# Kernel optimization log

Hardware: AMD Instinct MI355X
Metric: run time of the kernel (lower is better)

The kernel has to match this reference:

```python
import jax, jax.numpy as jnp
import numpy as np
from jax import lax

SQRT_HALF = np.float32(np.sqrt(0.5))


def glu_block(x, pad_mask, w, b):
    # x: [B,T,D], pad_mask: [B,T] True=padded, w: [2D,D,3], b: [2D]
    x = jnp.where(pad_mask[..., None], 0.0, x)
    xc = jnp.transpose(x, (0, 2, 1))  # [B,D,T]
    y = lax.conv_general_dilated(xc, w, (1,), 'SAME',
                                 dimension_numbers=('NCH', 'OIH', 'NCH'))
    y = y + b[None, :, None]
    y = jnp.transpose(y, (0, 2, 1))  # [B,T,2D]
    a, g = jnp.split(y, 2, axis=-1)
    out = a * jax.nn.sigmoid(g)
    return (out + x) * SQRT_HALF


def setup_inputs() -> dict:
    key = jax.random.key(0)
    ks = jax.random.split(key, 12)
    B, T_MEL, T_PH, D, V, MEL_D = 32, 2000, 512, 256, 100, 80
    mels = jax.random.normal(ks[0], (B, T_MEL, MEL_D), dtype=jnp.float32)
    phonemes = jax.random.randint(ks[1], (B, T_PH), 0, V)
    mel_lens = jax.random.randint(ks[2], (B,), 1, T_MEL)
    phoneme_lens = jax.random.randint(ks[3], (B,), 1, T_PH)
    embedding = 0.02 * jax.random.normal(ks[4], (V, D), dtype=jnp.float32)
    mel_conv_w = 0.02 * jax.random.normal(ks[5], (D, MEL_D, 3), dtype=jnp.float32)
    mel_conv_b = jnp.zeros((D,), dtype=jnp.float32)
    ph_w = 0.02 * jax.random.normal(ks[6], (4, 2 * D, D, 3), dtype=jnp.float32)
    ph_b = jnp.zeros((4, 2 * D), dtype=jnp.float32)
    mel_w = 0.02 * jax.random.normal(ks[7], (4, 2 * D, D, 3), dtype=jnp.float32)
    mel_b = jnp.zeros((4, 2 * D), dtype=jnp.float32)
    return {"mels": mels, "phonemes": phonemes, "mel_lens": mel_lens,
            "phoneme_lens": phoneme_lens, "embedding": embedding,
            "mel_conv_w": mel_conv_w, "mel_conv_b": mel_conv_b,
            "ph_w": ph_w, "ph_b": ph_b, "mel_w": mel_w, "mel_b": mel_b}


def reference(mels, phonemes, mel_lens, phoneme_lens, embedding,
              mel_conv_w, mel_conv_b, ph_w, ph_b, mel_w, mel_b):
    B, T_mel, _ = mels.shape
    # --- mel encoder ---
    mel_mask = jnp.arange(T_mel)[None, :] >= mel_lens[:, None]  # [B,T_mel]
    mc = lax.conv_general_dilated(jnp.transpose(mels, (0, 2, 1)), mel_conv_w,
                                  (1,), 'SAME',
                                  dimension_numbers=('NCH', 'OIH', 'NCH'))
    mel_enc = jnp.transpose(mc + mel_conv_b[None, :, None], (0, 2, 1))
    for i in range(4):
        mel_enc = glu_block(mel_enc, mel_mask, mel_w[i], mel_b[i])
    # --- phoneme encoder (prepend blank index 0) ---
    ph = jnp.pad(phonemes, ((0, 0), (1, 0)), constant_values=0)  # [B,T_ph+1]
    T_ph1 = ph.shape[1]
    ph_mask = jnp.arange(T_ph1)[None, :] > phoneme_lens[:, None]  # [B,T_ph+1]
    ph_enc = embedding[ph]  # [B,T_ph+1,D]
    for i in range(4):
        ph_enc = glu_block(ph_enc, ph_mask, ph_w[i], ph_b[i])
    # --- negative squared pairwise L2 distances, masked over padded phonemes ---
    mel_sq = jnp.sum(mel_enc * mel_enc, axis=-1)  # [B,T_mel]
    ph_sq = jnp.sum(ph_enc * ph_enc, axis=-1)     # [B,T_ph+1]
    dots = jnp.einsum('btd,bsd->bts', mel_enc, ph_enc)  # [B,T_mel,T_ph+1]
    distances = 2.0 * dots - mel_sq[:, :, None] - ph_sq[:, None, :]
    distances = jnp.where(ph_mask[:, None, :], -1e9, distances)
    attn = jax.nn.softmax(distances, axis=2)
    context = jnp.einsum('bts,bsd->btd', attn, ph_enc)
    return jnp.concatenate([mel_enc, context], axis=2)  # [B,T_mel,2D]
```

## Files before the change

### kernel.cpp

```cpp
#include <hip/hip_runtime.h>

typedef _Float16 f16;
typedef __attribute__((ext_vector_type(8))) _Float16 half8;
typedef __attribute__((ext_vector_type(4))) _Float16 half4;
typedef __attribute__((ext_vector_type(4))) float f32x4;

__device__ inline f32x4 mfma16(half8 a, half8 b, f32x4 c) {
  return __builtin_amdgcn_mfma_f32_16x16x32_f16(a, b, c, 0, 0, 0);
}

__global__ void prep_wtglu_kernel(const float* __restrict__ mel_w,
                                  const float* __restrict__ ph_w,
                                  f16* __restrict__ wt) {
  int bid = blockIdx.x;
  int l = bid >> 9, r = bid & 511;
  int tid = threadIdx.x;
  int n32 = r >> 5, j = r & 31;
  int ch = (j < 16) ? (n32 * 16 + j) : (256 + n32 * 16 + (j - 16));
  const float* src = ((l < 4) ? (mel_w + (size_t)l * 512 * 256 * 3)
                              : (ph_w + (size_t)(l - 4) * 512 * 256 * 3)) +
                     (size_t)ch * 768;
  f16* dst = wt + (size_t)bid * 768;
  float a0 = src[tid * 3], a1 = src[tid * 3 + 1], a2 = src[tid * 3 + 2];
  dst[tid] = (f16)a0;
  dst[256 + tid] = (f16)a1;
  dst[512 + tid] = (f16)a2;
}

__global__ void prep_wt0_kernel(const float* __restrict__ w, f16* __restrict__ wt0) {
  int idx = blockIdx.x * 256 + threadIdx.x;
  const int total = 256 * 288;
  if (idx >= total) return;
  int o = idx / 288, k = idx % 288;
  int tap = k / 96, i = k % 96;
  wt0[idx] = (i < 80) ? (f16)w[((size_t)o * 80 + i) * 3 + tap] : (f16)0.f;
}

__global__ void embed_kernel(const int* __restrict__ phon, const float* __restrict__ emb,
                             f16* __restrict__ out) {
  int s = blockIdx.x, b = blockIdx.y;
  int lane = threadIdx.x;
  int tok = (s == 0) ? 0 : phon[b * 512 + (s - 1)];
  float4 f = *(const float4*)(emb + (size_t)tok * 256 + lane * 4);
  half4 h = {(f16)f.x, (f16)f.y, (f16)f.z, (f16)f.w};
  *(half4*)(out + ((size_t)b * 513 + s) * 256 + lane * 4) = h;
}

__global__ __launch_bounds__(256) void conv0_kernel(
    const float* __restrict__ mels, const f16* __restrict__ wt0,
    const float* __restrict__ bias, f16* __restrict__ out) {
  __shared__ f16 xs[66 * 104];
  __shared__ f16 ws[64 * 104];
  const int tid = threadIdx.x;
  const int b = blockIdx.z;
  const int t0 = blockIdx.x * 64;
  const int by = blockIdx.y;

  for (int idx = tid; idx < 66 * 24; idx += 256) {
    int r = idx / 24, v = idx % 24;
    int t = t0 - 1 + r;
    half4 h = {0.f, 0.f, 0.f, 0.f};
    if (t >= 0 && t < 2000 && v < 20) {
      float4 f = *(const float4*)(mels + ((size_t)b * 2000 + t) * 80 + v * 4);
      h[0] = (f16)f.x; h[1] = (f16)f.y; h[2] = (f16)f.z; h[3] = (f16)f.w;
    }
    *(half4*)(xs + r * 104 + v * 4) = h;
  }
  const int lane = tid & 63, wv = tid >> 6;
  const int wr = wv >> 1, wc = wv & 1;
  const int l15 = lane & 15, q = lane >> 4;
  f32x4 acc[2][2] = {};
  const f16* wrow = wt0 + (size_t)(by * 64) * 288;
  for (int tap = 0; tap < 3; ++tap) {
    __syncthreads();
    for (int idx = tid; idx < 64 * 12; idx += 256) {
      int r = idx / 12, v = idx % 12;
      *(half8*)(ws + r * 104 + v * 8) =
          *(const half8*)(wrow + (size_t)r * 288 + tap * 96 + v * 8);
    }
    __syncthreads();
#pragma unroll
    for (int s2 = 0; s2 < 3; ++s2) {
      int ch = s2 * 32 + q * 8;
      half8 a0 = *(const half8*)(xs + (32 * wr + l15 + tap) * 104 + ch);
      half8 a1 = *(const half8*)(xs + (32 * wr + 16 + l15 + tap) * 104 + ch);
      half8 b0 = *(const half8*)(ws + (32 * wc + l15) * 104 + ch);
      half8 b1 = *(const half8*)(ws + (32 * wc + 16 + l15) * 104 + ch);
      acc[0][0] = mfma16(a0, b0, acc[0][0]);
      acc[0][1] = mfma16(a0, b1, acc[0][1]);
      acc[1][0] = mfma16(a1, b0, acc[1][0]);
      acc[1][1] = mfma16(a1, b1, acc[1][1]);
    }
  }
#pragma unroll
  for (int rf = 0; rf < 2; ++rf)
#pragma unroll
    for (int cf = 0; cf < 2; ++cf) {
      int c = by * 64 + 32 * wc + 16 * cf + l15;
      float bb = bias[c];
#pragma unroll
      for (int r = 0; r < 4; ++r) {
        int t = t0 + 32 * wr + 16 * rf + 4 * q + r;
        if (t < 2000)
          out[((size_t)b * 2000 + t) * 256 + c] = (f16)(acc[rf][cf][r] + bb);
      }
    }
}

__device__ __forceinline__ void glu_body(
    f16* xs, f16* ws2,
    const f16* __restrict__ x, const f16* __restrict__ wt,
    const float* __restrict__ bias, f16* __restrict__ out,
    const int* __restrict__ lens, int lenAdd, int T, int TT, int writeConst,
    int bx, int by, int b) {
  const int tid = threadIdx.x;
  const int tt = (bx + b) % TT;
  const int t0 = tt * 128;
  int thr = lens[b] + lenAdd;
  if (thr > T) thr = T;
  const size_t xbase = (size_t)b * T * 256;
  const int lane = tid & 63, wv = tid >> 6;
  const int wr = wv >> 1, wc = wv & 1;
  const int l15 = lane & 15, q = lane >> 4;

  if (t0 > thr) {
    if (writeConst) {
#pragma unroll
      for (int p = 0; p < 2; ++p) {
        int n32 = by * 4 + wc * 2 + p;
        int c = n32 * 16 + l15;
        float ba = bias[c], bg = bias[256 + c];
        f16 o = (f16)((ba * (1.0f / (1.0f + __expf(-bg)))) * 0.70710678118f);
#pragma unroll
        for (int mt = 0; mt < 4; ++mt)
#pragma unroll
          for (int rr = 0; rr < 4; ++rr) {
            int t = t0 + wr * 64 + mt * 16 + q * 4 + rr;
            if (t < T) out[xbase + (size_t)t * 256 + c] = o;
          }
      }
    }
    return;
  }

  f32x4 acc[4][4] = {};
  const f16* wrow = wt + (size_t)(by * 128) * 768;
  const int r_st = tid >> 3, v_st = tid & 7;

  half8 xr[5], wreg[4];
  auto loadX = [&](int cb) {
#pragma unroll
    for (int it = 0; it < 5; ++it) {
      int idx = tid + it * 256;
      half8 val = {};
      if (idx < 1040) {
        int lr = idx >> 3, v = idx & 7;
        int trow = t0 - 1 + lr;
        if (trow >= 0 && trow < thr)
          val = *(const half8*)(x + xbase + (size_t)trow * 256 + cb * 64 + v * 8);
      }
      xr[it] = val;
    }
  };
  auto storeX = [&]() {
#pragma unroll
    for (int it = 0; it < 5; ++it) {
      int idx = tid + it * 256;
      if (idx < 1040) {
        int lr = idx >> 3, v = idx & 7;
        *(half8*)(xs + lr * 72 + v * 8) = xr[it];
      }
    }
  };
  auto loadW = [&](int tap, int cb) {
#pragma unroll
    for (int it = 0; it < 4; ++it) {
      int r = r_st + 32 * it;
      wreg[it] = *(const half8*)(wrow + (size_t)r * 768 + tap * 256 + cb * 64 + v_st * 8);
    }
  };
  auto storeW = [&]() {
#pragma unroll
    for (int it = 0; it < 4; ++it)
      *(half8*)(ws2 + (r_st + 32 * it) * 72 + v_st * 8) = wreg[it];
  };

  loadX(0);
  loadW(0, 0);

  for (int p = 0; p < 12; ++p) {
    const int cb = p / 3, tap = p - cb * 3;
    __syncthreads();
    if (tap == 0) storeX();
    storeW();
    __syncthreads();
    if (p < 11) {
      int np = p + 1, ncb = np / 3, ntap = np - ncb * 3;
      if (ntap == 0) loadX(ncb);
      loadW(ntap, ncb);
    }

    half8 af[4][2];
#pragma unroll
    for (int mt = 0; mt < 4; ++mt)
#pragma unroll
      for (int kc = 0; kc < 2; ++kc)
        af[mt][kc] = *(const half8*)(xs + (wr * 64 + mt * 16 + l15 + tap) * 72 + kc * 32 + q * 8);
#pragma unroll
    for (int nt = 0; nt < 4; ++nt) {
      half8 b0 = *(const half8*)(ws2 + (wc * 64 + nt * 16 + l15) * 72 + q * 8);
      half8 b1 = *(const half8*)(ws2 + (wc * 64 + nt * 16 + l15) * 72 + 32 + q * 8);
#pragma unroll
      for (int mt = 0; mt < 4; ++mt) {
        acc[mt][nt] = mfma16(af[mt][0], b0, acc[mt][nt]);
        acc[mt][nt] = mfma16(af[mt][1], b1, acc[mt][nt]);
      }
    }
  }

#pragma unroll
  for (int p = 0; p < 2; ++p) {
    int n32 = by * 4 + wc * 2 + p;
    int c = n32 * 16 + l15;
    float ba = bias[c], bg = bias[256 + c];
#pragma unroll
    for (int mt = 0; mt < 4; ++mt) {
#pragma unroll
      for (int rr = 0; rr < 4; ++rr) {
        int t = t0 + wr * 64 + mt * 16 + q * 4 + rr;
        if (t < T && (writeConst || t < thr)) {
          float a = acc[mt][2 * p][rr] + ba;
          float g = acc[mt][2 * p + 1][rr] + bg;
          float xm = (t < thr) ? (float)x[xbase + (size_t)t * 256 + c] : 0.f;
          float o = (a * (1.0f / (1.0f + __expf(-g))) + xm) * 0.70710678118f;
          out[xbase + (size_t)t * 256 + c] = (f16)o;
        }
      }
    }
  }
}

__global__ __launch_bounds__(256) void glu_fused_kernel(
    const f16* __restrict__ xm, const f16* __restrict__ wtm,
    const float* __restrict__ bm, f16* __restrict__ om,
    const int* __restrict__ mlens,
    const f16* __restrict__ xp, const f16* __restrict__ wtp,
    const float* __restrict__ bp, f16* __restrict__ op,
    const int* __restrict__ plens, int writeConst) {
  __shared__ f16 xs[132 * 72];
  __shared__ f16 ws2[128 * 72];
  const int lin = blockIdx.x;
  if (lin < 2048) {
    int b = lin >> 6, y = (lin >> 4) & 3, x = lin & 15;
    glu_body(xs, ws2, xm, wtm, bm, om, mlens, 0, 2000, 16, writeConst, x, y, b);
  } else {
    int l2 = lin - 2048;
    int b = l2 / 20, r = l2 % 20, y = r / 5, x = r % 5;
    glu_body(xs, ws2, xp, wtp, bp, op, plens, 1, 513, 5, writeConst, x, y, b);
  }
}

__global__ __launch_bounds__(256) void transpose_kernel(const f16* __restrict__ ph,
                                                        f16* __restrict__ phT) {
  __shared__ f16 tile[64 * 72];
  const int tid = threadIdx.x;
  const int b = blockIdx.z, s0 = blockIdx.x * 64, d0 = blockIdx.y * 64;
#pragma unroll
  for (int it = 0; it < 2; ++it) {
    int idx = tid + it * 256;
    int r = idx >> 3, v = idx & 7;
    int s = s0 + r;
    half8 val = {};
    if (s < 513) val = *(const half8*)(ph + ((size_t)b * 513 + s) * 256 + d0 + v * 8);
    *(half8*)(tile + r * 72 + v * 8) = val;
  }
  __syncthreads();
#pragma unroll
  for (int it = 0; it < 2; ++it) {
    int idx = tid + it * 256;
    int r = idx >> 3, v = idx & 7;
    half8 val;
#pragma unroll
    for (int j2 = 0; j2 < 8; ++j2) val[j2] = tile[(v * 8 + j2) * 72 + r];
    *(half8*)(phT + ((size_t)b * 256 + d0 + r) * 576 + s0 + v * 8) = val;
  }
}

__global__ void sqnorm_kernel(const f16* __restrict__ x, float* __restrict__ sq, int nrows) {
  int row = blockIdx.x * 4 + (threadIdx.x >> 6);
  int lane = threadIdx.x & 63;
  if (row >= nrows) return;
  const f16* p = x + (size_t)row * 256;
  float v = 0.f;
  for (int i = lane; i < 256; i += 64) { float f = (float)p[i]; v += f * f; }
  for (int off = 32; off > 0; off >>= 1) v += __shfl_down(v, off);
  if (lane == 0) sq[row] = v;
}

__global__ __launch_bounds__(256) void flash_kernel(
    const f16* __restrict__ mel, const f16* __restrict__ ph,
    const f16* __restrict__ phT, const float* __restrict__ phsq,
    const int* __restrict__ plens, float* __restrict__ out) {
  __shared__ f16 vt[256 * 72];
  __shared__ f16 ps[4][16 * 72];
  __shared__ float phs[576];
  const int tid = threadIdx.x;
  const int lin = blockIdx.x;
  const int b = ((lin >> 8) << 3) | (lin & 7);
  const int t0 = ((lin >> 3) & 31) * 64;
  const int lane = tid & 63, wv = tid >> 6;
  const int l15 = lane & 15, q = lane >> 4;
  const int plen = plens[b];
  const int nkt = (plen + 64) >> 6;

  for (int idx = tid; idx < 576; idx += 256)
    phs[idx] = (idx < 513) ? phsq[b * 513 + idx] : 0.f;

  const int tq = t0 + 16 * wv + l15;
  half8 qf[8];
  {
    const f16* qrow = mel + ((size_t)b * 2000 + ((tq < 2000) ? tq : 0)) * 256;
#pragma unroll
    for (int c = 0; c < 8; ++c) qf[c] = *(const half8*)(qrow + c * 32 + q * 8);
    if (tq >= 2000) {
      half8 z = {};
#pragma unroll
      for (int c = 0; c < 8; ++c) qf[c] = z;
    }
  }
  if (tq < 2000) {
    float* orow = out + ((size_t)b * 2000 + tq) * 512;
#pragma unroll
    for (int c = 0; c < 8; ++c) {
      half8 h = qf[c];
      float4 f0 = {(float)h[0], (float)h[1], (float)h[2], (float)h[3]};
      float4 f1 = {(float)h[4], (float)h[5], (float)h[6], (float)h[7]};
      *(float4*)(orow + c * 32 + q * 8) = f0;
      *(float4*)(orow + c * 32 + q * 8 + 4) = f1;
    }
  }

  half8 vreg[8];
  const int d_st = tid >> 3, v_st = tid & 7;
  auto loadV = [&](int kt) {
#pragma unroll
    for (int it = 0; it < 8; ++it) {
      int d = d_st + 32 * it;
      vreg[it] = *(const half8*)(phT + ((size_t)b * 256 + d) * 576 + kt * 64 + v_st * 8);
    }
  };
  loadV(0);

  float mr[4], lr[4];
#pragma unroll
  for (int r = 0; r < 4; ++r) { mr[r] = -3.0e38f; lr[r] = 0.f; }
  f32x4 acc[16] = {};
  f16* pw = ps[wv];

#pragma unroll 1
  for (int kt = 0; kt < nkt; ++kt) {
    const int s0 = kt * 64;
    __syncthreads();
#pragma unroll
    for (int it = 0; it < 8; ++it)
      *(half8*)(vt + (d_st + 32 * it) * 72 + v_st * 8) = vreg[it];
    __syncthreads();
    if (kt + 1 < nkt) loadV(kt + 1);

    const f16* krow[4];
#pragma unroll
    for (int cf = 0; cf < 4; ++cf)
      krow[cf] = ph + ((size_t)b * 513 + (s0 + cf * 16 + l15)) * 256 + q * 8;
    f32x4 sc[4] = {};
    __builtin_amdgcn_s_setprio(1);
#pragma unroll
    for (int c = 0; c < 8; ++c) {
#pragma unroll
      for (int cf = 0; cf < 4; ++cf) {
        half8 bf = *(const half8*)(krow[cf] + c * 32);
        sc[cf] = mfma16(qf[c], bf, sc[cf]);
      }
    }
    __builtin_amdgcn_s_setprio(0);
    float p[4][4];
    float rmax[4] = {-3.0e38f, -3.0e38f, -3.0e38f, -3.0e38f};
#pragma unroll
    for (int cf = 0; cf < 4; ++cf) {
      int sloc = cf * 16 + l15;
      int s = s0 + sloc;
      bool msk = (s > plen) || (s >= 513);
      float p2 = phs[s0 + sloc];
#pragma unroll
      for (int r = 0; r < 4; ++r) {
        float v = 2.0f * sc[cf][r] - p2;
        if (msk) v = -1.0e9f;
        p[cf][r] = v;
        rmax[r] = fmaxf(rmax[r], v);
      }
    }
#pragma unroll
    for (int r = 0; r < 4; ++r)
#pragma unroll
      for (int off = 1; off < 16; off <<= 1)
        rmax[r] = fmaxf(rmax[r], __shfl_xor(rmax[r], off));
    float alpha[4];
#pragma unroll
    for (int r = 0; r < 4; ++r) {
      float mn = fmaxf(mr[r], rmax[r]);
      alpha[r] = __expf(mr[r] - mn);
      mr[r] = mn;
      float rs = 0.f;
#pragma unroll
      for (int cf = 0; cf < 4; ++cf) {
        float e = __expf(p[cf][r] - mn);
        p[cf][r] = e;
        rs += e;
      }
#pragma unroll
      for (int off = 1; off < 16; off <<= 1) rs += __shfl_xor(rs, off);
      lr[r] = lr[r] * alpha[r] + rs;
    }
#pragma unroll
    for (int dt = 0; dt < 16; ++dt)
#pragma unroll
      for (int r = 0; r < 4; ++r) acc[dt][r] *= alpha[r];
#pragma unroll
    for (int cf = 0; cf < 4; ++cf)
#pragma unroll
      for (int r = 0; r < 4; ++r)
        pw[(q * 4 + r) * 72 + cf * 16 + l15] = (f16)p[cf][r];
#pragma unroll
    for (int kc = 0; kc < 2; ++kc) {
      half8 pa = *(const half8*)(pw + l15 * 72 + kc * 32 + q * 8);
      __builtin_amdgcn_s_setprio(1);
#pragma unroll
      for (int dt = 0; dt < 16; ++dt) {
        half8 vb = *(const half8*)(vt + (dt * 16 + l15) * 72 + kc * 32 + q * 8);
        acc[dt] = mfma16(pa, vb, acc[dt]);
      }
      __builtin_amdgcn_s_setprio(0);
    }
  }
  float inv[4];
#pragma unroll
  for (int r = 0; r < 4; ++r) inv[r] = 1.0f / lr[r];
#pragma unroll
  for (int dt = 0; dt < 16; ++dt)
#pragma unroll
    for (int r = 0; r < 4; ++r) {
      int t = t0 + 16 * wv + q * 4 + r;
      if (t < 2000) {
        int d = dt * 16 + l15;
        out[((size_t)b * 2000 + t) * 512 + 256 + d] = acc[dt][r] * inv[r];
      }
    }
}

extern "C" void kernel_launch(void* const* d_in, const int* in_sizes, int n_in,
                              void* d_out, int out_size, void* d_ws, size_t ws_size,
                              hipStream_t stream) {
  (void)in_sizes; (void)n_in; (void)out_size; (void)ws_size;
  const float* mels       = (const float*)d_in[0];
  const int*   phonemes   = (const int*)d_in[1];
  const int*   mel_lens   = (const int*)d_in[2];
  const int*   ph_lens    = (const int*)d_in[3];
  const float* embedding  = (const float*)d_in[4];
  const float* mel_conv_w = (const float*)d_in[5];
  const float* mel_conv_b = (const float*)d_in[6];
  const float* ph_w       = (const float*)d_in[7];
  const float* ph_b       = (const float*)d_in[8];
  const float* mel_w      = (const float*)d_in[9];
  const float* mel_b      = (const float*)d_in[10];
  float* out = (float*)d_out;

  char* wsp = (char*)d_ws;
  size_t off = 0;
  auto alloc = [&](size_t bytes) -> void* {
    void* p = wsp + off;
    off = (off + bytes + 255) & ~(size_t)255;
    return p;
  };
  f16* wtg    = (f16*)alloc(8ull * 512 * 768 * 2);
  f16* wt0    = (f16*)alloc(256ull * 288 * 2);
  float* phsq = (float*)alloc(16416ull * 4);
  f16* p0     = (f16*)alloc(32ull * 513 * 256 * 2);
  f16* p1     = (f16*)alloc(32ull * 513 * 256 * 2);
  f16* m0     = (f16*)alloc(32ull * 2000 * 256 * 2);
  f16* m1     = (f16*)alloc(32ull * 2000 * 256 * 2);
  f16* phT = m1;

  prep_wtglu_kernel<<<4096, 256, 0, stream>>>(mel_w, ph_w, wtg);
  prep_wt0_kernel<<<288, 256, 0, stream>>>(mel_conv_w, wt0);
  embed_kernel<<<dim3(513, 32), 64, 0, stream>>>(phonemes, embedding, p0);
  conv0_kernel<<<dim3(32, 4, 32), 256, 0, stream>>>(mels, wt0, mel_conv_b, m0);

  const size_t WL = 512ull * 768;
  glu_fused_kernel<<<2688, 256, 0, stream>>>(
      m0, wtg + 0 * WL, mel_b + 0 * 512, m1, mel_lens,
      p0, wtg + 4 * WL, ph_b + 0 * 512, p1, ph_lens, 0);
  glu_fused_kernel<<<2688, 256, 0, stream>>>(
      m1, wtg + 1 * WL, mel_b + 1 * 512, m0, mel_lens,
      p1, wtg + 5 * WL, ph_b + 1 * 512, p0, ph_lens, 0);
  glu_fused_kernel<<<2688, 256, 0, stream>>>(
      m0, wtg + 2 * WL, mel_b + 2 * 512, m1, mel_lens,
      p0, wtg + 6 * WL, ph_b + 2 * 512, p1, ph_lens, 0);
  glu_fused_kernel<<<2688, 256, 0, stream>>>(
      m1, wtg + 3 * WL, mel_b + 3 * 512, m0, mel_lens,
      p1, wtg + 7 * WL, ph_b + 3 * 512, p0, ph_lens, 1);

  transpose_kernel<<<dim3(9, 4, 32), 256, 0, stream>>>(p0, phT);
  sqnorm_kernel<<<4104, 256, 0, stream>>>(p0, phsq, 16416);
  flash_kernel<<<dim3(32 * 32), 256, 0, stream>>>(m0, p0, phT, phsq, ph_lens, out);
}
```

Baseline: 658.2 us.

## Pre-swizzle GLU weights into MFMA fragment order and load directly to registers

```diff
diff --git a/kernel.cpp b/kernel.cpp
--- a/kernel.cpp
+++ b/kernel.cpp
@@ -13,18 +13,26 @@
                                   const float* __restrict__ ph_w,
                                   f16* __restrict__ wt) {
   int bid = blockIdx.x;
-  int l = bid >> 9, r = bid & 511;
+  int p = bid % 12, lby = bid / 12;
+  int by = lby & 3, l = lby >> 2;
+  int cb = p / 3, tap = p - cb * 3;
+  const float* src = (l < 4) ? (mel_w + (size_t)l * 512 * 256 * 3)
+                             : (ph_w + (size_t)(l - 4) * 512 * 256 * 3);
+  f16* dst = wt + (size_t)bid * 8192;
   int tid = threadIdx.x;
-  int n32 = r >> 5, j = r & 31;
-  int ch = (j < 16) ? (n32 * 16 + j) : (256 + n32 * 16 + (j - 16));
-  const float* src = ((l < 4) ? (mel_w + (size_t)l * 512 * 256 * 3)
-                              : (ph_w + (size_t)(l - 4) * 512 * 256 * 3)) +
-                     (size_t)ch * 768;
-  f16* dst = wt + (size_t)bid * 768;
-  float a0 = src[tid * 3], a1 = src[tid * 3 + 1], a2 = src[tid * 3 + 2];
-  dst[tid] = (f16)a0;
-  dst[256 + tid] = (f16)a1;
-  dst[512 + tid] = (f16)a2;
+#pragma unroll
+  for (int k = 0; k < 4; ++k) {
+    int s = tid + k * 256;
+    int lane = s & 63, rest = s >> 6;
+    int kc = rest & 1, nt = (rest >> 1) & 3, wc = rest >> 3;
+    int rg = by * 128 + wc * 64 + nt * 16 + (lane & 15);
+    int n32 = rg >> 5, j = rg & 31;
+    int ch = (j < 16) ? (n32 * 16 + j) : (256 + n32 * 16 + (j - 16));
+    int i0 = cb * 64 + kc * 32 + (lane >> 4) * 8;
+#pragma unroll
+    for (int e = 0; e < 8; ++e)
+      dst[(size_t)s * 8 + e] = (f16)src[((size_t)ch * 256 + i0 + e) * 3 + tap];
+  }
 }
 
 __global__ void prep_wt0_kernel(const float* __restrict__ w, f16* __restrict__ wt0) {
@@ -108,7 +116,7 @@
 }
 
 __device__ __forceinline__ void glu_body(
-    f16* xs, f16* ws2,
+    f16* xs,
     const f16* __restrict__ x, const f16* __restrict__ wt,
     const float* __restrict__ bias, f16* __restrict__ out,
     const int* __restrict__ lens, int lenAdd, int T, int TT, int writeConst,
@@ -144,10 +152,10 @@
   }
 
   f32x4 acc[4][4] = {};
-  const f16* wrow = wt + (size_t)(by * 128) * 768;
-  const int r_st = tid >> 3, v_st = tid & 7;
-
-  half8 xr[5], wreg[4];
+  const f16* wby = wt + (size_t)by * 12 * 8192 + (size_t)wc * 4096 + (size_t)lane * 8;
+
+  half8 xr[5];
+  half8 wb[4][2], wn[4][2];
   auto loadX = [&](int cb) {
 #pragma unroll
     for (int it = 0; it < 5; ++it) {
@@ -172,48 +180,48 @@
       }
     }
   };
-  auto loadW = [&](int tap, int cb) {
-#pragma unroll
-    for (int it = 0; it < 4; ++it) {
-      int r = r_st + 32 * it;
-      wreg[it] = *(const half8*)(wrow + (size_t)r * 768 + tap * 256 + cb * 64 + v_st * 8);
-    }
+  auto loadWreg = [&](half8 W[4][2], int p) {
+    const f16* wp = wby + (size_t)p * 8192;
+#pragma unroll
+    for (int nt = 0; nt < 4; ++nt)
+#pragma unroll
+      for (int kc = 0; kc < 2; ++kc)
+        W[nt][kc] = *(const half8*)(wp + (nt * 2 + kc) * 512);
   };
-  auto storeW = [&]() {
-#pragma unroll
-    for (int it = 0; it < 4; ++it)
-      *(half8*)(ws2 + (r_st + 32 * it) * 72 + v_st * 8) = wreg[it];
-  };
 
   loadX(0);
-  loadW(0, 0);
-
-  for (int p = 0; p < 12; ++p) {
-    const int cb = p / 3, tap = p - cb * 3;
+  loadWreg(wb, 0);
+
+#pragma unroll
+  for (int cb = 0; cb < 4; ++cb) {
     __syncthreads();
-    if (tap == 0) storeX();
-    storeW();
+    storeX();
     __syncthreads();
-    if (p < 11) {
-      int np = p + 1, ncb = np / 3, ntap = np - ncb * 3;
-      if (ntap == 0) loadX(ncb);
-      loadW(ntap, ncb);
-    }
-
-    half8 af[4][2];
-#pragma unroll
-    for (int mt = 0; mt < 4; ++mt)
-#pragma unroll
-      for (int kc = 0; kc < 2; ++kc)
-        af[mt][kc] = *(const half8*)(xs + (wr * 64 + mt * 16 + l15 + tap) * 72 + kc * 32 + q * 8);
-#pragma unroll
-    for (int nt = 0; nt < 4; ++nt) {
-      half8 b0 = *(const half8*)(ws2 + (wc * 64 + nt * 16 + l15) * 72 + q * 8);
-      half8 b1 = *(const half8*)(ws2 + (wc * 64 + nt * 16 + l15) * 72 + 32 + q * 8);
-#pragma unroll
-      for (int mt = 0; mt < 4; ++mt) {
-        acc[mt][nt] = mfma16(af[mt][0], b0, acc[mt][nt]);
-        acc[mt][nt] = mfma16(af[mt][1], b1, acc[mt][nt]);
+    if (cb < 3) loadX(cb + 1);
+#pragma unroll
+    for (int tap = 0; tap < 3; ++tap) {
+      const int p = cb * 3 + tap;
+      if (p < 11) loadWreg(wn, p + 1);
+
+      half8 af[4][2];
+#pragma unroll
+      for (int mt = 0; mt < 4; ++mt)
+#pragma unroll
+        for (int kc = 0; kc < 2; ++kc)
+          af[mt][kc] = *(const half8*)(xs + (wr * 64 + mt * 16 + l15 + tap) * 72 + kc * 32 + q * 8);
+      __builtin_amdgcn_s_setprio(1);
+#pragma unroll
+      for (int nt = 0; nt < 4; ++nt)
+#pragma unroll
+        for (int mt = 0; mt < 4; ++mt) {
+          acc[mt][nt] = mfma16(af[mt][0], wb[nt][0], acc[mt][nt]);
+          acc[mt][nt] = mfma16(af[mt][1], wb[nt][1], acc[mt][nt]);
+        }
+      __builtin_amdgcn_s_setprio(0);
+#pragma unroll
+      for (int nt = 0; nt < 4; ++nt) {
+        wb[nt][0] = wn[nt][0];
+        wb[nt][1] = wn[nt][1];
       }
     }
   }
@@ -248,15 +256,14 @@
     const float* __restrict__ bp, f16* __restrict__ op,
     const int* __restrict__ plens, int writeConst) {
   __shared__ f16 xs[132 * 72];
-  __shared__ f16 ws2[128 * 72];
   const int lin = blockIdx.x;
   if (lin < 2048) {
     int b = lin >> 6, y = (lin >> 4) & 3, x = lin & 15;
-    glu_body(xs, ws2, xm, wtm, bm, om, mlens, 0, 2000, 16, writeConst, x, y, b);
+    glu_body(xs, xm, wtm, bm, om, mlens, 0, 2000, 16, writeConst, x, y, b);
   } else {
     int l2 = lin - 2048;
     int b = l2 / 20, r = l2 % 20, y = r / 5, x = r % 5;
-    glu_body(xs, ws2, xp, wtp, bp, op, plens, 1, 513, 5, writeConst, x, y, b);
+    glu_body(xs, xp, wtp, bp, op, plens, 1, 513, 5, writeConst, x, y, b);
   }
 }
 
@@ -480,7 +487,7 @@
     off = (off + bytes + 255) & ~(size_t)255;
     return p;
   };
-  f16* wtg    = (f16*)alloc(8ull * 512 * 768 * 2);
+  f16* wtg    = (f16*)alloc(8ull * 4 * 12 * 8192 * 2);
   f16* wt0    = (f16*)alloc(256ull * 288 * 2);
   float* phsq = (float*)alloc(16416ull * 4);
   f16* p0     = (f16*)alloc(32ull * 513 * 256 * 2);
@@ -489,12 +496,12 @@
   f16* m1     = (f16*)alloc(32ull * 2000 * 256 * 2);
   f16* phT = m1;
 
-  prep_wtglu_kernel<<<4096, 256, 0, stream>>>(mel_w, ph_w, wtg);
+  prep_wtglu_kernel<<<384, 256, 0, stream>>>(mel_w, ph_w, wtg);
   prep_wt0_kernel<<<288, 256, 0, stream>>>(mel_conv_w, wt0);
   embed_kernel<<<dim3(513, 32), 64, 0, stream>>>(phonemes, embedding, p0);
   conv0_kernel<<<dim3(32, 4, 32), 256, 0, stream>>>(mels, wt0, mel_conv_b, m0);
 
-  const size_t WL = 512ull * 768;
+  const size_t WL = 4ull * 12 * 8192;
   glu_fused_kernel<<<2688, 256, 0, stream>>>(
       m0, wtg + 0 * WL, mel_b + 0 * 512, m1, mel_lens,
       p0, wtg + 4 * WL, ph_b + 0 * 512, p1, ph_lens, 0);
```

Result: faster. 614.5 us (-6.6%).
